# Kernel optimization log

Hardware: AMD Instinct MI355X
Metric: run time of the kernel (lower is better)

Reference implementation:

```python
import jax, jax.numpy as jnp
import numpy as np

N_NODES = 15
EMBED_DIM = 2048
F1 = 1024
F2 = 512
N_EDGES = 120


def gcn_conv(x, src, dst, W, b):
    # PyG GCNConv: h = D^{-1/2} (A + I) D^{-1/2} (x W) + b
    h = x @ W                                   # [N, F_out]
    n = h.shape[0]
    loops = jnp.arange(n)
    s = jnp.concatenate([src, loops])
    d = jnp.concatenate([dst, loops])
    deg = jax.ops.segment_sum(jnp.ones_like(d, dtype=h.dtype), d, num_segments=n)
    dinv = jax.lax.rsqrt(deg)                   # deg >= 1 due to self loops
    norm = dinv[s] * dinv[d]                    # [E+N]
    out = jax.ops.segment_sum(h[s] * norm[:, None], d, num_segments=n)
    return out + b


def attention_pool(x, attW):
    # SimGNN-style attention: global ctx = tanh(mean(x W)); scores = sigmoid(x @ ctx)
    ctx = jnp.tanh(jnp.mean(x @ attW, axis=0))  # [F2]
    scores = jax.nn.sigmoid(x @ ctx)            # [N]
    return x.T @ scores                         # [F2]


def setup_inputs() -> dict:
    key = jax.random.key(0)
    ks = jax.random.split(key, 16)
    d = {}
    d['features_1'] = jax.random.normal(ks[0], (N_NODES,), dtype=jnp.float32)
    d['edge_index_1'] = jax.random.randint(ks[1], (2, N_EDGES), 0, N_NODES, dtype=jnp.int32)
    d['target'] = jax.random.uniform(ks[2], (3,), dtype=jnp.float32)
    def lin(k, fi, fo):
        s = 1.0 / np.sqrt(fi)
        kw, kb = jax.random.split(k)
        return (jax.random.uniform(kw, (fi, fo), minval=-s, maxval=s, dtype=jnp.float32),
                jax.random.uniform(kb, (fo,), minval=-s, maxval=s, dtype=jnp.float32))
    d['W1'], d['b1'] = lin(ks[3], 15, 15 * 32)
    d['W2'], d['b2'] = lin(ks[4], 15 * 32, 15 * 128)
    d['W3'], d['b3'] = lin(ks[5], 15 * 128, 15 * EMBED_DIM)
    d['gW1'], d['gb1'] = lin(ks[6], EMBED_DIM, F1)
    d['gW2'], d['gb2'] = lin(ks[7], F1, F2)
    d['attW'] = jax.random.normal(ks[8], (F2, F2), dtype=jnp.float32) * (1.0 / np.sqrt(F2))
    d['fcW'], d['fcb'] = lin(ks[9], F2, 3)
    return d


def reference(features_1, edge_index_1, target, W1, b1, W2, b2, W3, b3,
              gW1, gb1, gW2, gb2, attW, fcW, fcb):
    # embed MLP: 15 -> 480 -> 1920 -> 15*embed_dim
    h = jax.nn.relu(features_1 @ W1 + b1)
    h = jax.nn.relu(h @ W2 + b2)
    h = (h @ W3 + b3).reshape(N_NODES, EMBED_DIM)
    src, dst = edge_index_1[0], edge_index_1[1]
    x = jax.nn.relu(gcn_conv(h, src, dst, gW1, gb1))
    x = gcn_conv(x, src, dst, gW2, gb2)
    rep = attention_pool(x, attW)               # [F2]
    logits = rep @ fcW + fcb                    # [3]
    cls = jnp.argmax(target)
    loss = -jax.nn.log_softmax(logits)[cls]
    predictions = jax.nn.softmax(logits)
    return loss, predictions
```

## Files before the change

### kernel.cpp

```cpp
#include <hip/hip_runtime.h>
#include <math.h>

#define NN 15
#define EMBED 2048
#define F1D 1024
#define F2D 512
#define NE 120
#define H1_DIM 480
#define H2_DIM 1920
#define H3_DIM 30720

#define OFF_A    0
#define OFF_H2   256
#define OFF_P3   2304
#define OFF_XG1  248064
#define OFF_P1   278784
#define OFF_XG2  524544
#define OFF_P2   539904
#define OFF_X2   662784
#define OFF_XBAR 670464
#define OFF_CTX  670976

__device__ inline void f4ma(float4& a, float s, const float4& w) {
    a.x += s * w.x; a.y += s * w.y; a.z += s * w.z; a.w += s * w.w;
}
__device__ inline void f4acc(float4& a, const float4& b) {
    a.x += b.x; a.y += b.y; a.z += b.z; a.w += b.w;
}

__global__ void k1_h2(const float* __restrict__ f, const float* __restrict__ W1,
                      const float* __restrict__ b1, const float* __restrict__ W2,
                      const float* __restrict__ b2, const int* __restrict__ edges,
                      float* __restrict__ ws) {
    int tid = threadIdx.x;
    if (blockIdx.x == 60) {
        __shared__ float dinv[NN];
        __shared__ float A[NN * NN];
        if (tid < NN) {
            int deg = 1;
            for (int i = 0; i < NE; ++i) deg += (edges[NE + i] == tid) ? 1 : 0;
            dinv[tid] = rsqrtf((float)deg);
        }
        __syncthreads();
        if (tid < NN * NN) {
            int r = tid / NN, c = tid % NN;
            A[tid] = (r == c) ? dinv[r] * dinv[r] : 0.0f;
        }
        __syncthreads();
        if (tid == 0) {
            for (int i = 0; i < NE; ++i) {
                int s = edges[i], d = edges[NE + i];
                A[d * NN + s] += dinv[s] * dinv[d];
            }
        }
        __syncthreads();
        if (tid < NN * NN) ws[OFF_A + tid] = A[tid];
        return;
    }
    __shared__ float h1[H1_DIM];
    __shared__ float4 red[32][8];
    float fr[NN];
#pragma unroll
    for (int k = 0; k < NN; ++k) fr[k] = f[k];
    for (int j = tid; j < H1_DIM; j += 256) {
        float acc = b1[j];
#pragma unroll
        for (int k = 0; k < NN; ++k) acc += fr[k] * W1[k * H1_DIM + j];
        h1[j] = fmaxf(acc, 0.0f);
    }
    __syncthreads();
    int jg = tid & 7, kc = tid >> 3;
    int j = blockIdx.x * 32 + jg * 4;
    float4 acc = make_float4(0.f, 0.f, 0.f, 0.f);
    for (int r = 0; r < 15; ++r) {
        int k = kc * 15 + r;
        float4 w = *(const float4*)(W2 + k * H2_DIM + j);
        f4ma(acc, h1[k], w);
    }
    red[kc][jg] = acc;
    __syncthreads();
    for (int s = 16; s >= 1; s >>= 1) {
        if (kc < s) f4acc(red[kc][jg], red[kc + s][jg]);
        __syncthreads();
    }
    if (kc == 0) {
        float4 b = *(const float4*)(b2 + j);
        float4 v = red[0][jg];
        v.x = fmaxf(v.x + b.x, 0.f); v.y = fmaxf(v.y + b.y, 0.f);
        v.z = fmaxf(v.z + b.z, 0.f); v.w = fmaxf(v.w + b.w, 0.f);
        *(float4*)(ws + OFF_H2 + j) = v;
    }
}

__global__ void k2_h3(const float* __restrict__ W3, float* __restrict__ ws) {
    __shared__ float h2l[240];
    __shared__ float4 red[128];
    int tid = threadIdx.x;
    int cb = blockIdx.x, kc = blockIdx.y;
    int kbase = kc * 240;
    for (int i = tid; i < 240; i += 256) h2l[i] = ws[OFF_H2 + kbase + i];
    __syncthreads();
    int f4i = tid & 127, rg = tid >> 7;
    int col = cb * 512 + f4i * 4;
    float4 acc = make_float4(0.f, 0.f, 0.f, 0.f);
    const float* wp = W3 + (size_t)(kbase + rg) * H3_DIM + col;
#pragma unroll 8
    for (int i = 0; i < 120; ++i) {
        float4 w = *(const float4*)wp;
        f4ma(acc, h2l[2 * i + rg], w);
        wp += 2 * (size_t)H3_DIM;
    }
    if (rg == 1) red[f4i] = acc;
    __syncthreads();
    if (rg == 0) {
        f4acc(acc, red[f4i]);
        *(float4*)(ws + OFF_P3 + (size_t)kc * H3_DIM + col) = acc;
    }
}

__global__ void k3_agg1(const float* __restrict__ b3, float* __restrict__ ws) {
    __shared__ float Al[NN * NN];
    __shared__ float S[NN][32];
    int tid = threadIdx.x;
    int c0 = blockIdx.x * 32;
    for (int i = tid; i < NN * NN; i += 256) Al[i] = ws[OFF_A + i];
    for (int q = tid; q < NN * 32; q += 256) {
        int m = q >> 5, c = q & 31;
        int j = m * EMBED + c0 + c;
        float s = b3[j];
#pragma unroll
        for (int p = 0; p < 8; ++p) s += ws[OFF_P3 + p * H3_DIM + j];
        S[m][c] = s;
    }
    __syncthreads();
    for (int q = tid; q < NN * 32; q += 256) {
        int n = q >> 5, c = q & 31;
        float x = 0.f;
#pragma unroll
        for (int m = 0; m < NN; ++m) x += Al[n * NN + m] * S[m][c];
        ws[OFF_XG1 + n * EMBED + c0 + c] = x;
    }
}

template<int IN, int OUT, int ECH>
__global__ void k_mmP(const float* __restrict__ X, const float* __restrict__ W,
                      float* __restrict__ P) {
    __shared__ float Xl[NN * ECH];
    __shared__ float4 red[8][32][NN];
    int tid = threadIdx.x;
    int e0 = blockIdx.y * ECH;
    for (int i = tid; i < NN * ECH; i += 256) {
        int n = i / ECH, e = i - n * ECH;
        Xl[i] = X[n * IN + e0 + e];
    }
    __syncthreads();
    int fg = tid & 31, kt = tid >> 5;
    int f = blockIdx.x * 128 + fg * 4;
    float4 acc[NN];
#pragma unroll
    for (int n = 0; n < NN; ++n) acc[n] = make_float4(0.f, 0.f, 0.f, 0.f);
    const int RPT = ECH / 8;
    for (int r = 0; r < RPT; ++r) {
        int e = kt * RPT + r;
        float4 w = *(const float4*)(W + (size_t)(e0 + e) * OUT + f);
#pragma unroll
        for (int n = 0; n < NN; ++n) f4ma(acc[n], Xl[n * ECH + e], w);
    }
    __syncthreads();
#pragma unroll
    for (int n = 0; n < NN; ++n) red[kt][fg][n] = acc[n];
    __syncthreads();
    for (int s = 4; s >= 1; s >>= 1) {
        if (kt < s) {
#pragma unroll
            for (int n = 0; n < NN; ++n) f4acc(red[kt][fg][n], red[kt + s][fg][n]);
        }
        __syncthreads();
    }
    if (kt == 0) {
#pragma unroll
        for (int n = 0; n < NN; ++n) {
            float4 v = red[0][fg][n];
            *(float4*)(P + (size_t)blockIdx.y * NN * OUT + n * OUT + f) = v;
        }
    }
}

__global__ void k5_fin1(const float* __restrict__ gb1, float* __restrict__ ws) {
    __shared__ float Al[NN * NN];
    __shared__ float S[NN][64];
    int tid = threadIdx.x;
    int f0 = blockIdx.x * 64;
    for (int i = tid; i < NN * NN; i += 256) Al[i] = ws[OFF_A + i];
    for (int q = tid; q < NN * 64; q += 256) {
        int n = q >> 6, c = q & 63;
        float s = gb1[f0 + c];
#pragma unroll
        for (int p = 0; p < 16; ++p) s += ws[OFF_P1 + p * (NN * F1D) + n * F1D + f0 + c];
        S[n][c] = fmaxf(s, 0.f);
    }
    __syncthreads();
    for (int q = tid; q < NN * 64; q += 256) {
        int n = q >> 6, c = q & 63;
        float x = 0.f;
#pragma unroll
        for (int m = 0; m < NN; ++m) x += Al[n * NN + m] * S[m][c];
        ws[OFF_XG2 + n * F1D + f0 + c] = x;
    }
}

__global__ void k7_fin2(const float* __restrict__ gb2, float* __restrict__ ws) {
    __shared__ float S[NN][64];
    int tid = threadIdx.x;
    int f0 = blockIdx.x * 64;
    for (int q = tid; q < NN * 64; q += 256) {
        int n = q >> 6, c = q & 63;
        float s = gb2[f0 + c];
#pragma unroll
        for (int p = 0; p < 16; ++p) s += ws[OFF_P2 + p * (NN * F2D) + n * F2D + f0 + c];
        S[n][c] = s;
        ws[OFF_X2 + n * F2D + f0 + c] = s;
    }
    __syncthreads();
    if (tid < 64) {
        float s = 0.f;
#pragma unroll
        for (int n = 0; n < NN; ++n) s += S[n][tid];
        ws[OFF_XBAR + f0 + tid] = s * (1.0f / 15.0f);
    }
}

__global__ void k8_ctx(const float* __restrict__ attW, float* __restrict__ ws) {
    __shared__ float xb[F2D];
    __shared__ float4 red[64][4];
    int tid = threadIdx.x;
    for (int e = tid; e < F2D; e += 256) xb[e] = ws[OFF_XBAR + e];
    __syncthreads();
    int fg = tid & 3, kt = tid >> 2;
    int f = blockIdx.x * 16 + fg * 4;
    float4 acc = make_float4(0.f, 0.f, 0.f, 0.f);
    for (int r = 0; r < 8; ++r) {
        int e = kt * 8 + r;
        float4 w = *(const float4*)(attW + e * F2D + f);
        f4ma(acc, xb[e], w);
    }
    red[kt][fg] = acc;
    __syncthreads();
    for (int s = 32; s >= 1; s >>= 1) {
        if (kt < s) f4acc(red[kt][fg], red[kt + s][fg]);
        __syncthreads();
    }
    if (kt == 0) {
        float4 v = red[0][fg];
        ws[OFF_CTX + f + 0] = tanhf(v.x);
        ws[OFF_CTX + f + 1] = tanhf(v.y);
        ws[OFF_CTX + f + 2] = tanhf(v.z);
        ws[OFF_CTX + f + 3] = tanhf(v.w);
    }
}

__global__ void k9_final(const float* __restrict__ fcW, const float* __restrict__ fcb,
                         const float* __restrict__ target, const float* __restrict__ ws,
                         float* __restrict__ out) {
    __shared__ float x2l[NN * F2D];
    __shared__ float ctxl[F2D];
    __shared__ float scores[16];
    __shared__ float rep[F2D];
    __shared__ float logits[3];
    int tid = threadIdx.x;
    for (int i = tid; i < NN * F2D; i += 256) x2l[i] = ws[OFF_X2 + i];
    for (int i = tid; i < F2D; i += 256) ctxl[i] = ws[OFF_CTX + i];
    __syncthreads();
    {
        int g = tid >> 4, l = tid & 15;
        if (g < NN) {
            float p = 0.f;
            for (int i = 0; i < 32; ++i) {
                int e = l + 16 * i;
                p += x2l[g * F2D + e] * ctxl[e];
            }
            p += __shfl_xor(p, 1); p += __shfl_xor(p, 2);
            p += __shfl_xor(p, 4); p += __shfl_xor(p, 8);
            if (l == 0) scores[g] = 1.0f / (1.0f + expf(-p));
        }
    }
    __syncthreads();
    for (int fi = tid; fi < F2D; fi += 256) {
        float v = 0.f;
#pragma unroll
        for (int n = 0; n < NN; ++n) v += x2l[n * F2D + fi] * scores[n];
        rep[fi] = v;
    }
    __syncthreads();
    if (tid < 192) {
        int j = tid >> 6, l = tid & 63;
        float p = 0.f;
        for (int i = 0; i < 8; ++i) {
            int e = l + 64 * i;
            p += rep[e] * fcW[e * 3 + j];
        }
        p += __shfl_xor(p, 1); p += __shfl_xor(p, 2); p += __shfl_xor(p, 4);
        p += __shfl_xor(p, 8); p += __shfl_xor(p, 16); p += __shfl_xor(p, 32);
        if (l == 0) logits[j] = p + fcb[j];
    }
    __syncthreads();
    if (tid == 0) {
        float t0 = target[0], t1 = target[1], t2 = target[2];
        int cls = 0; float best = t0;
        if (t1 > best) { best = t1; cls = 1; }
        if (t2 > best) { cls = 2; }
        float l0 = logits[0], l1 = logits[1], l2 = logits[2];
        float m = fmaxf(l0, fmaxf(l1, l2));
        float e0 = expf(l0 - m), e1 = expf(l1 - m), e2 = expf(l2 - m);
        float s = e0 + e1 + e2;
        float lc = (cls == 0) ? l0 : ((cls == 1) ? l1 : l2);
        out[0] = -(lc - m - logf(s));
        out[1] = e0 / s; out[2] = e1 / s; out[3] = e2 / s;
    }
}

extern "C" void kernel_launch(void* const* d_in, const int* in_sizes, int n_in,
                              void* d_out, int out_size, void* d_ws, size_t ws_size,
                              hipStream_t stream) {
    const float* f    = (const float*)d_in[0];
    const int*   ei   = (const int*)d_in[1];
    const float* tgt  = (const float*)d_in[2];
    const float* W1   = (const float*)d_in[3];
    const float* b1   = (const float*)d_in[4];
    const float* W2   = (const float*)d_in[5];
    const float* b2   = (const float*)d_in[6];
    const float* W3   = (const float*)d_in[7];
    const float* b3   = (const float*)d_in[8];
    const float* gW1  = (const float*)d_in[9];
    const float* gb1  = (const float*)d_in[10];
    const float* gW2  = (const float*)d_in[11];
    const float* gb2  = (const float*)d_in[12];
    const float* attW = (const float*)d_in[13];
    const float* fcW  = (const float*)d_in[14];
    const float* fcb  = (const float*)d_in[15];
    float* ws  = (float*)d_ws;
    float* out = (float*)d_out;

    k1_h2<<<dim3(61), dim3(256), 0, stream>>>(f, W1, b1, W2, b2, ei, ws);
    k2_h3<<<dim3(60, 8), dim3(256), 0, stream>>>(W3, ws);
    k3_agg1<<<dim3(64), dim3(256), 0, stream>>>(b3, ws);
    k_mmP<2048, 1024, 128><<<dim3(8, 16), dim3(256), 0, stream>>>(ws + OFF_XG1, gW1, ws + OFF_P1);
    k5_fin1<<<dim3(16), dim3(256), 0, stream>>>(gb1, ws);
    k_mmP<1024, 512, 64><<<dim3(4, 16), dim3(256), 0, stream>>>(ws + OFF_XG2, gW2, ws + OFF_P2);
    k7_fin2<<<dim3(8), dim3(256), 0, stream>>>(gb2, ws);
    k8_ctx<<<dim3(32), dim3(256), 0, stream>>>(attW, ws);
    k9_final<<<dim3(1), dim3(256), 0, stream>>>(fcW, fcb, tgt, ws, out);
}
```

Measured before the change: 411.0 us.

## Fuse partial reductions and adjacency aggregation into GCN matmul kernels; resplit W3 GEMV

The partial-sum reduction, bias, ReLU and normalized-adjacency aggregation stages are folded into the prologue of the two GCN matmul kernels. This removes two separate kernel launches and the round-trip of the intermediate aggregated features through global memory. The W3 GEMV is also resplit into 32 K-chunks of 60 rows with 512 threads per block, so each block keeps its full partial and needs no in-block reduction. The trade-off is that every column block of the fused kernels now redundantly re-reads and reduces all partials for its input slice. There are also four times as many partial buffers for the first layer to sum.

```diff
diff --git a/kernel.cpp b/kernel.cpp
--- a/kernel.cpp
+++ b/kernel.cpp
@@ -13,13 +13,11 @@
 #define OFF_A    0
 #define OFF_H2   256
 #define OFF_P3   2304
-#define OFF_XG1  248064
-#define OFF_P1   278784
-#define OFF_XG2  524544
-#define OFF_P2   539904
-#define OFF_X2   662784
-#define OFF_XBAR 670464
-#define OFF_CTX  670976
+#define OFF_P1   985344
+#define OFF_P2   1231104
+#define OFF_X2   1353984
+#define OFF_XBAR 1361664
+#define OFF_CTX  1362176
 
 __device__ inline void f4ma(float4& a, float s, const float4& w) {
     a.x += s * w.x; a.y += s * w.y; a.z += s * w.z; a.w += s * w.w;
@@ -93,66 +91,56 @@
 }
 
 __global__ void k2_h3(const float* __restrict__ W3, float* __restrict__ ws) {
-    __shared__ float h2l[240];
-    __shared__ float4 red[128];
+    __shared__ float h2l[60];
     int tid = threadIdx.x;
     int cb = blockIdx.x, kc = blockIdx.y;
-    int kbase = kc * 240;
-    for (int i = tid; i < 240; i += 256) h2l[i] = ws[OFF_H2 + kbase + i];
-    __syncthreads();
-    int f4i = tid & 127, rg = tid >> 7;
-    int col = cb * 512 + f4i * 4;
+    int kbase = kc * 60;
+    if (tid < 60) h2l[tid] = ws[OFF_H2 + kbase + tid];
+    __syncthreads();
+    int col = cb * 2048 + tid * 4;
     float4 acc = make_float4(0.f, 0.f, 0.f, 0.f);
-    const float* wp = W3 + (size_t)(kbase + rg) * H3_DIM + col;
-#pragma unroll 8
-    for (int i = 0; i < 120; ++i) {
+    const float* wp = W3 + (size_t)kbase * H3_DIM + col;
+#pragma unroll 6
+    for (int r = 0; r < 60; ++r) {
         float4 w = *(const float4*)wp;
-        f4ma(acc, h2l[2 * i + rg], w);
-        wp += 2 * (size_t)H3_DIM;
-    }
-    if (rg == 1) red[f4i] = acc;
-    __syncthreads();
-    if (rg == 0) {
-        f4acc(acc, red[f4i]);
-        *(float4*)(ws + OFF_P3 + (size_t)kc * H3_DIM + col) = acc;
-    }
-}
-
-__global__ void k3_agg1(const float* __restrict__ b3, float* __restrict__ ws) {
+        f4ma(acc, h2l[r], w);
+        wp += (size_t)H3_DIM;
+    }
+    *(float4*)(ws + OFF_P3 + (size_t)kc * H3_DIM + col) = acc;
+}
+
+template<int IN, int OUT, int ECH, int NPART, bool BIAS_PER_NODE, bool RELU>
+__global__ void k_mmA(const float* __restrict__ P, const float* __restrict__ bias,
+                      const float* __restrict__ W, const float* __restrict__ wsA,
+                      float* __restrict__ Pout) {
+    __shared__ float4 red[8][32][NN];
+    __shared__ float Xl[NN * ECH];
     __shared__ float Al[NN * NN];
-    __shared__ float S[NN][32];
-    int tid = threadIdx.x;
-    int c0 = blockIdx.x * 32;
-    for (int i = tid; i < NN * NN; i += 256) Al[i] = ws[OFF_A + i];
-    for (int q = tid; q < NN * 32; q += 256) {
-        int m = q >> 5, c = q & 31;
-        int j = m * EMBED + c0 + c;
-        float s = b3[j];
-#pragma unroll
-        for (int p = 0; p < 8; ++p) s += ws[OFF_P3 + p * H3_DIM + j];
-        S[m][c] = s;
-    }
-    __syncthreads();
-    for (int q = tid; q < NN * 32; q += 256) {
-        int n = q >> 5, c = q & 31;
+    float* S = (float*)red;
+    int tid = threadIdx.x;
+    int e0 = blockIdx.y * ECH;
+    for (int i = tid; i < NN * NN; i += 256) Al[i] = wsA[i];
+    for (int q = tid; q < NN * ECH; q += 256) {
+        int m = q / ECH, c = q - m * ECH;
+        float s = BIAS_PER_NODE ? bias[m * IN + e0 + c] : bias[e0 + c];
+#pragma unroll
+        for (int p = 0; p < NPART; ++p) s += P[(size_t)p * NN * IN + m * IN + e0 + c];
+        if (RELU) s = fmaxf(s, 0.f);
+        S[q] = s;
+    }
+    __syncthreads();
+    float xtmp[8];
+    int nq = 0;
+    for (int q = tid; q < NN * ECH; q += 256, ++nq) {
+        int n = q / ECH, c = q - n * ECH;
         float x = 0.f;
 #pragma unroll
-        for (int m = 0; m < NN; ++m) x += Al[n * NN + m] * S[m][c];
-        ws[OFF_XG1 + n * EMBED + c0 + c] = x;
-    }
-}
-
-template<int IN, int OUT, int ECH>
-__global__ void k_mmP(const float* __restrict__ X, const float* __restrict__ W,
-                      float* __restrict__ P) {
-    __shared__ float Xl[NN * ECH];
-    __shared__ float4 red[8][32][NN];
-    int tid = threadIdx.x;
-    int e0 = blockIdx.y * ECH;
-    for (int i = tid; i < NN * ECH; i += 256) {
-        int n = i / ECH, e = i - n * ECH;
-        Xl[i] = X[n * IN + e0 + e];
-    }
+        for (int m = 0; m < NN; ++m) x += Al[n * NN + m] * S[m * ECH + c];
+        xtmp[nq] = x;
+    }
+    __syncthreads();
+    nq = 0;
+    for (int q = tid; q < NN * ECH; q += 256, ++nq) Xl[q] = xtmp[nq];
     __syncthreads();
     int fg = tid & 31, kt = tid >> 5;
     int f = blockIdx.x * 128 + fg * 4;
@@ -180,32 +168,8 @@
     if (kt == 0) {
 #pragma unroll
         for (int n = 0; n < NN; ++n) {
-            float4 v = red[0][fg][n];
-            *(float4*)(P + (size_t)blockIdx.y * NN * OUT + n * OUT + f) = v;
-        }
-    }
-}
-
-__global__ void k5_fin1(const float* __restrict__ gb1, float* __restrict__ ws) {
-    __shared__ float Al[NN * NN];
-    __shared__ float S[NN][64];
-    int tid = threadIdx.x;
-    int f0 = blockIdx.x * 64;
-    for (int i = tid; i < NN * NN; i += 256) Al[i] = ws[OFF_A + i];
-    for (int q = tid; q < NN * 64; q += 256) {
-        int n = q >> 6, c = q & 63;
-        float s = gb1[f0 + c];
-#pragma unroll
-        for (int p = 0; p < 16; ++p) s += ws[OFF_P1 + p * (NN * F1D) + n * F1D + f0 + c];
-        S[n][c] = fmaxf(s, 0.f);
-    }
-    __syncthreads();
-    for (int q = tid; q < NN * 64; q += 256) {
-        int n = q >> 6, c = q & 63;
-        float x = 0.f;
-#pragma unroll
-        for (int m = 0; m < NN; ++m) x += Al[n * NN + m] * S[m][c];
-        ws[OFF_XG2 + n * F1D + f0 + c] = x;
+            *(float4*)(Pout + (size_t)blockIdx.y * NN * OUT + n * OUT + f) = red[0][fg][n];
+        }
     }
 }
 
@@ -342,11 +306,11 @@
     float* out = (float*)d_out;
 
     k1_h2<<<dim3(61), dim3(256), 0, stream>>>(f, W1, b1, W2, b2, ei, ws);
-    k2_h3<<<dim3(60, 8), dim3(256), 0, stream>>>(W3, ws);
-    k3_agg1<<<dim3(64), dim3(256), 0, stream>>>(b3, ws);
-    k_mmP<2048, 1024, 128><<<dim3(8, 16), dim3(256), 0, stream>>>(ws + OFF_XG1, gW1, ws + OFF_P1);
-    k5_fin1<<<dim3(16), dim3(256), 0, stream>>>(gb1, ws);
-    k_mmP<1024, 512, 64><<<dim3(4, 16), dim3(256), 0, stream>>>(ws + OFF_XG2, gW2, ws + OFF_P2);
+    k2_h3<<<dim3(15, 32), dim3(512), 0, stream>>>(W3, ws);
+    k_mmA<2048, 1024, 128, 32, true, false>
+        <<<dim3(8, 16), dim3(256), 0, stream>>>(ws + OFF_P3, b3, gW1, ws + OFF_A, ws + OFF_P1);
+    k_mmA<1024, 512, 64, 16, false, true>
+        <<<dim3(4, 16), dim3(256), 0, stream>>>(ws + OFF_P1, gb1, gW2, ws + OFF_A, ws + OFF_P2);
     k7_fin2<<<dim3(8), dim3(256), 0, stream>>>(gb2, ws);
     k8_ctx<<<dim3(32), dim3(256), 0, stream>>>(attW, ws);
     k9_final<<<dim3(1), dim3(256), 0, stream>>>(fcW, fcb, tgt, ws, out);
```

New measurement: 421.2 us. 2.5% more time.
